# Optimization experiments

Measured on AMD Instinct MI355X. Metric: run time of the kernel, lower is better.

Reference implementation:

```python
import jax, jax.numpy as jnp
import numpy as np

BATCH = 1024
NUM_GENES = 20000          # output_dimension == cfg['num_genes']
NONGENE_DIM = 64           # input_dimension - output_dimension
EMB_DIM = 32               # cfg['gene_embedding_size']
INPUT_DIM = NUM_GENES + NONGENE_DIM
FC_IN = NONGENE_DIM + 1 + EMB_DIM  # concat(nongene, x_j, emb_j)


def setup_inputs() -> dict:
    key = jax.random.key(0)
    k1, k2, k3, k4 = jax.random.split(key, 4)
    x = jax.random.normal(k1, (BATCH, INPUT_DIM), dtype=jnp.float32)
    # nn.Embedding default init: N(0,1)
    emb = jax.random.normal(k2, (NUM_GENES, EMB_DIM), dtype=jnp.float32)
    # nn.Linear(FC_IN, 1): weight [1, FC_IN] U(-1/sqrt(in), 1/sqrt(in)); flatten to [FC_IN]
    bound = 1.0 / np.sqrt(FC_IN)
    W = jax.random.uniform(k3, (FC_IN,), dtype=jnp.float32, minval=-bound, maxval=bound)
    b = jax.random.uniform(k4, (), dtype=jnp.float32, minval=-bound, maxval=bound)
    return {"x": x, "emb": emb, "W": W, "b": b}


def reference(x, emb, W, b):
    # Original loop: y[:, j] = fc(concat(nongene, x[:, j:j+1], emb[j].repeat(B,1)))
    # fc weight splits into [W_ng | w_x | W_e]; the linear is separable:
    #   y[b, j] = nongene[b] . W_ng + x[b, j] * w_x + emb[j] . W_e + bias
    G, E = emb.shape
    D_ng = W.shape[0] - 1 - E
    nongene = x[:, -D_ng:]                       # [B, D_ng]
    W_ng, w_x, W_e = W[:D_ng], W[D_ng], W[D_ng + 1:]
    ng_term = nongene @ W_ng                     # [B]  constant across genes
    gene_term = emb @ W_e                        # [G]  constant across batch
    y = ng_term[:, None] + x[:, :G] * w_x + gene_term[None, :] + b  # [B, G]
    return y
```

## Files before the change

### kernel.cpp

```cpp
#include <hip/hip_runtime.h>

#define BATCH 1024
#define NUM_GENES 20000
#define NONGENE_DIM 64
#define EMB_DIM 32
#define INPUT_DIM (NUM_GENES + NONGENE_DIM)
#define G4 (NUM_GENES / 4)

__global__ void dlge_precompute(const float* __restrict__ x,
                                const float* __restrict__ emb,
                                const float* __restrict__ W,
                                float* __restrict__ ws) {
    const int tid = blockIdx.x * blockDim.x + threadIdx.x;
    if (tid < NUM_GENES) {
        const float4* e4 = reinterpret_cast<const float4*>(emb + (size_t)tid * EMB_DIM);
        float acc = 0.0f;
#pragma unroll
        for (int k = 0; k < EMB_DIM / 4; ++k) {
            const float4 e = e4[k];
            acc += e.x * W[NONGENE_DIM + 1 + 4 * k + 0]
                 + e.y * W[NONGENE_DIM + 1 + 4 * k + 1]
                 + e.z * W[NONGENE_DIM + 1 + 4 * k + 2]
                 + e.w * W[NONGENE_DIM + 1 + 4 * k + 3];
        }
        ws[tid] = acc;
    } else if (tid < NUM_GENES + BATCH) {
        const int row = tid - NUM_GENES;
        const float4* n4 = reinterpret_cast<const float4*>(
            x + (size_t)row * INPUT_DIM + NUM_GENES);
        float acc = 0.0f;
#pragma unroll
        for (int k = 0; k < NONGENE_DIM / 4; ++k) {
            const float4 v = n4[k];
            acc += v.x * W[4 * k + 0] + v.y * W[4 * k + 1]
                 + v.z * W[4 * k + 2] + v.w * W[4 * k + 3];
        }
        ws[NUM_GENES + row] = acc;
    }
}

__global__ void dlge_main(const float* __restrict__ x,
                          const float* __restrict__ ws,
                          const float* __restrict__ W,
                          const float* __restrict__ bptr,
                          float* __restrict__ y) {
    const int row = blockIdx.y;
    const int j = blockIdx.x * blockDim.x + threadIdx.x;
    if (j >= G4) return;

    const float wx = W[NONGENE_DIM];
    const float s  = ws[NUM_GENES + row] + bptr[0];

    const float4 x4 = reinterpret_cast<const float4*>(x + (size_t)row * INPUT_DIM)[j];
    const float4 g4 = reinterpret_cast<const float4*>(ws)[j];

    float4 o;
    o.x = s + x4.x * wx + g4.x;
    o.y = s + x4.y * wx + g4.y;
    o.z = s + x4.z * wx + g4.z;
    o.w = s + x4.w * wx + g4.w;

    reinterpret_cast<float4*>(y + (size_t)row * NUM_GENES)[j] = o;
}

extern "C" void kernel_launch(void* const* d_in, const int* in_sizes, int n_in,
                              void* d_out, int out_size, void* d_ws, size_t ws_size,
                              hipStream_t stream) {
    const float* x   = (const float*)d_in[0];
    const float* emb = (const float*)d_in[1];
    const float* W   = (const float*)d_in[2];
    const float* b   = (const float*)d_in[3];
    float* y  = (float*)d_out;
    float* ws = (float*)d_ws;

    {
        const int total = NUM_GENES + BATCH;
        const int blocks = (total + 255) / 256;
        dlge_precompute<<<blocks, 256, 0, stream>>>(x, emb, W, ws);
    }

    {
        dim3 grid((G4 + 255) / 256, BATCH);
        dlge_main<<<grid, 256, 0, stream>>>(x, ws, W, b, y);
    }
}
```

Baseline: 33.82 us.

## Fuse precompute into main kernel with row-blocked gene tiles

Merges the two kernels into one. Each block covers a 1000-gene tile across 32 batch rows. It computes the gene embedding dot products in registers and the nongene row sums in shared memory using a shuffle reduction, then streams x to y for all 32 rows. This removes a kernel launch and the workspace round trip, at the cost of recomputing the embedding terms once per row group (32 times in total) and leaving 6 of 256 threads idle in the main loop.

```diff
diff --git a/kernel.cpp b/kernel.cpp
--- a/kernel.cpp
+++ b/kernel.cpp
@@ -5,62 +5,87 @@
 #define NONGENE_DIM 64
 #define EMB_DIM 32
 #define INPUT_DIM (NUM_GENES + NONGENE_DIM)
-#define G4 (NUM_GENES / 4)
+#define ROWS_PER_BLOCK 32
+#define TILE_GENES 1024
+#define N_TILES (NUM_GENES / TILE_GENES)
 
-__global__ void dlge_precompute(const float* __restrict__ x,
-                                const float* __restrict__ emb,
-                                const float* __restrict__ W,
-                                float* __restrict__ ws) {
-    const int tid = blockIdx.x * blockDim.x + threadIdx.x;
-    if (tid < NUM_GENES) {
-        const float4* e4 = reinterpret_cast<const float4*>(emb + (size_t)tid * EMB_DIM);
-        float acc = 0.0f;
-#pragma unroll
-        for (int k = 0; k < EMB_DIM / 4; ++k) {
-            const float4 e = e4[k];
-            acc += e.x * W[NONGENE_DIM + 1 + 4 * k + 0]
-                 + e.y * W[NONGENE_DIM + 1 + 4 * k + 1]
-                 + e.z * W[NONGENE_DIM + 1 + 4 * k + 2]
-                 + e.w * W[NONGENE_DIM + 1 + 4 * k + 3];
-        }
-        ws[tid] = acc;
-    } else if (tid < NUM_GENES + BATCH) {
-        const int row = tid - NUM_GENES;
+#undef TILE_GENES
+#define TILE_GENES 1000
+#define TILE_F4 (TILE_GENES / 4)
+
+__global__ __launch_bounds__(256)
+void dlge_fused(const float* __restrict__ x,
+                const float* __restrict__ emb,
+                const float* __restrict__ W,
+                const float* __restrict__ bptr,
+                float* __restrict__ y) {
+    __shared__ float s_ng[ROWS_PER_BLOCK];
+
+    const int t    = threadIdx.x;
+    const int tile = blockIdx.x;
+    const int rowg = blockIdx.y;
+    const int row0 = rowg * ROWS_PER_BLOCK;
+
+    {
+        const int r = t >> 3;
+        const int k = t & 7;
+        const int row = row0 + r;
         const float4* n4 = reinterpret_cast<const float4*>(
             x + (size_t)row * INPUT_DIM + NUM_GENES);
-        float acc = 0.0f;
+        const float4 a = n4[k];
+        const float4 c = n4[k + 8];
+        float p = a.x * W[4 * k + 0] + a.y * W[4 * k + 1]
+                + a.z * W[4 * k + 2] + a.w * W[4 * k + 3]
+                + c.x * W[32 + 4 * k + 0] + c.y * W[32 + 4 * k + 1]
+                + c.z * W[32 + 4 * k + 2] + c.w * W[32 + 4 * k + 3];
+        p += __shfl_down(p, 4, 8);
+        p += __shfl_down(p, 2, 8);
+        p += __shfl_down(p, 1, 8);
+        if (k == 0) s_ng[r] = p + bptr[0];
+    }
+
+    const bool active = (t < TILE_F4);
+    const int g0 = tile * TILE_GENES + t * 4;
+    float gt0 = 0.f, gt1 = 0.f, gt2 = 0.f, gt3 = 0.f;
+    if (active) {
+        float acc[4];
 #pragma unroll
-        for (int k = 0; k < NONGENE_DIM / 4; ++k) {
-            const float4 v = n4[k];
-            acc += v.x * W[4 * k + 0] + v.y * W[4 * k + 1]
-                 + v.z * W[4 * k + 2] + v.w * W[4 * k + 3];
+        for (int q = 0; q < 4; ++q) {
+            const float4* e4 = reinterpret_cast<const float4*>(
+                emb + (size_t)(g0 + q) * EMB_DIM);
+            float a = 0.f;
+#pragma unroll
+            for (int k = 0; k < EMB_DIM / 4; ++k) {
+                const float4 e = e4[k];
+                a += e.x * W[NONGENE_DIM + 1 + 4 * k + 0]
+                   + e.y * W[NONGENE_DIM + 1 + 4 * k + 1]
+                   + e.z * W[NONGENE_DIM + 1 + 4 * k + 2]
+                   + e.w * W[NONGENE_DIM + 1 + 4 * k + 3];
+            }
+            acc[q] = a;
         }
-        ws[NUM_GENES + row] = acc;
+        gt0 = acc[0]; gt1 = acc[1]; gt2 = acc[2]; gt3 = acc[3];
     }
-}
 
-__global__ void dlge_main(const float* __restrict__ x,
-                          const float* __restrict__ ws,
-                          const float* __restrict__ W,
-                          const float* __restrict__ bptr,
-                          float* __restrict__ y) {
-    const int row = blockIdx.y;
-    const int j = blockIdx.x * blockDim.x + threadIdx.x;
-    if (j >= G4) return;
+    __syncthreads();
 
+    if (!active) return;
     const float wx = W[NONGENE_DIM];
-    const float s  = ws[NUM_GENES + row] + bptr[0];
+    const int j = tile * TILE_F4 + t;
 
-    const float4 x4 = reinterpret_cast<const float4*>(x + (size_t)row * INPUT_DIM)[j];
-    const float4 g4 = reinterpret_cast<const float4*>(ws)[j];
-
-    float4 o;
-    o.x = s + x4.x * wx + g4.x;
-    o.y = s + x4.y * wx + g4.y;
-    o.z = s + x4.z * wx + g4.z;
-    o.w = s + x4.w * wx + g4.w;
-
-    reinterpret_cast<float4*>(y + (size_t)row * NUM_GENES)[j] = o;
+#pragma unroll 8
+    for (int r = 0; r < ROWS_PER_BLOCK; ++r) {
+        const int row = row0 + r;
+        const float s = s_ng[r];
+        const float4 x4 = reinterpret_cast<const float4*>(
+            x + (size_t)row * INPUT_DIM)[j];
+        float4 o;
+        o.x = s + x4.x * wx + gt0;
+        o.y = s + x4.y * wx + gt1;
+        o.z = s + x4.z * wx + gt2;
+        o.w = s + x4.w * wx + gt3;
+        reinterpret_cast<float4*>(y + (size_t)row * NUM_GENES)[j] = o;
+    }
 }
 
 extern "C" void kernel_launch(void* const* d_in, const int* in_sizes, int n_in,
@@ -70,17 +95,8 @@
     const float* emb = (const float*)d_in[1];
     const float* W   = (const float*)d_in[2];
     const float* b   = (const float*)d_in[3];
-    float* y  = (float*)d_out;
-    float* ws = (float*)d_ws;
+    float* y = (float*)d_out;
 
-    {
-        const int total = NUM_GENES + BATCH;
-        const int blocks = (total + 255) / 256;
-        dlge_precompute<<<blocks, 256, 0, stream>>>(x, emb, W, ws);
-    }
-
-    {
-        dim3 grid((G4 + 255) / 256, BATCH);
-        dlge_main<<<grid, 256, 0, stream>>>(x, ws, W, b, y);
-    }
+    dim3 grid(NUM_GENES / TILE_GENES, BATCH / ROWS_PER_BLOCK);
+    dlge_fused<<<grid, 256, 0, stream>>>(x, emb, W, b, y);
 }
```

Measured after the change: 58.25 us. 72.3% more time.
